# Kernel tuning notes

Hardware: AMD Instinct MI355X
Metric: run time of the kernel (lower is better)

Reference implementation:

```python
import jax, jax.numpy as jnp
import numpy as np

ALPHA = 0.2          # LeakyReLU negative slope
NEG = -9e15          # masking value from the torch source


def _gat_multihead(x, adj, W, a):
    """All nheads GATLayers (concat=True math, elu applied by caller).
    x: [B,N,F], adj: [B,N,N], W: [H,F,O], a: [H,2O]. Returns [B,H,N,O].
    Note a_input @ a decomposes as h_i.a[:O] + h_j.a[O:], so we never
    materialize the O(N^2 * 2O) pairwise concat tensor."""
    h = jnp.einsum('bnf,hfo->bhno', x, W)            # [B,H,N,O]
    O = h.shape[-1]
    s1 = jnp.einsum('bhno,ho->bhn', h, a[:, :O])     # h_i . a_src
    s2 = jnp.einsum('bhno,ho->bhn', h, a[:, O:])     # h_j . a_dst
    e = jax.nn.leaky_relu(s1[..., :, None] + s2[..., None, :], ALPHA)  # [B,H,N,N]
    att = jax.nn.softmax(jnp.where(adj[:, None] > 0, e, NEG), axis=-1)
    return jnp.einsum('bhij,bhjo->bhio', att, h)


def _gat_single(x, adj, W, a):
    """out_att GATLayer (concat=False, no elu). W: [F,O], a: [2O]."""
    h = jnp.einsum('bnf,fo->bno', x, W)
    O = W.shape[-1]
    s1 = h @ a[:O]
    s2 = h @ a[O:]
    e = jax.nn.leaky_relu(s1[:, :, None] + s2[:, None, :], ALPHA)
    att = jax.nn.softmax(jnp.where(adj > 0, e, NEG), axis=-1)
    return jnp.einsum('bij,bjo->bio', att, h)


def setup_inputs() -> dict:
    key = jax.random.key(0)
    ks = jax.random.split(key, 10)
    B, N, F = 2, 2048, 768
    H, O = 8, 256
    x = jax.random.normal(ks[0], (B, N, F), dtype=jnp.float32)
    # sparse-ish binary adjacency (adj>0 is all that matters) + self loops
    adj = (jax.random.uniform(ks[1], (B, N, N)) < 0.05).astype(jnp.float32)
    adj = jnp.maximum(adj, jnp.eye(N, dtype=jnp.float32)[None])
    mask = jnp.ones((B, N, 1), dtype=jnp.float32)  # unused by GAT.forward
    s = 0.05
    W_heads = jax.random.normal(ks[2], (H, F, O), dtype=jnp.float32) * s
    a_heads = jax.random.normal(ks[3], (H, 2 * O), dtype=jnp.float32) * s
    W_out = jax.random.normal(ks[4], (H * O, O), dtype=jnp.float32) * s
    a_out = jax.random.normal(ks[5], (2 * O,), dtype=jnp.float32) * s
    W_lin = jax.random.normal(ks[6], (O, H * O), dtype=jnp.float32) * s  # nn.Linear weight [out,in]
    b_lin = jnp.zeros((O,), dtype=jnp.float32)
    W_ln = jax.random.normal(ks[7], (O, O), dtype=jnp.float32) * s
    b_ln = jnp.zeros((O,), dtype=jnp.float32)
    return {"x": x, "adj": adj, "mask": mask, "W_heads": W_heads,
            "a_heads": a_heads, "W_out": W_out, "a_out": a_out,
            "W_lin": W_lin, "b_lin": b_lin, "W_ln": W_ln, "b_ln": b_ln}


def reference(x, adj, mask, W_heads, a_heads, W_out, a_out, W_lin, b_lin, W_ln, b_ln):
    # layer 0: multi-head GAT, elu, concat over heads (dropout=0 in eval)
    hp = jax.nn.elu(_gat_multihead(x, adj, W_heads, a_heads))  # [B,H,N,O]
    B, H, N, O = hp.shape
    x1 = jnp.transpose(hp, (0, 2, 1, 3)).reshape(B, N, H * O)
    # layer 1: residual linear + out_att (concat=False)
    x2 = x1 @ W_lin.T + b_lin + _gat_single(x1, adj, W_out, a_out)
    # final: relu(ln(x))
    return jax.nn.relu(x2 @ W_ln.T + b_ln)
```

## Files before the change

kernel.cpp:

```cpp
#include <hip/hip_runtime.h>
#include <hip/hip_bf16.h>

constexpr int Bb = 2, Nn = 2048, Ff = 768, Hh = 8, Oo = 256;

typedef __attribute__((ext_vector_type(8)))  short   short8;
typedef __attribute__((ext_vector_type(16))) float   f32x16;
typedef __attribute__((ext_vector_type(4)))  unsigned short ushort4_t;

__device__ inline unsigned short f2bf(float f) {
    unsigned u = __float_as_uint(f);
    u = (u + 0x7FFFu + ((u >> 16) & 1u)) >> 16;
    return (unsigned short)u;
}

__device__ inline void wfrag_kn_body(
        const float* __restrict__ W, unsigned short* __restrict__ out,
        int K, int N, int fblk, int t) {
    int f = fblk * 4 + (t >> 6);
    int slot = t & 63, kh = slot >> 5, lm = slot & 31;
    int nfk = K >> 4;
    int nt = f / nfk, kt = f - nt * nfk;
    const float* wp = W + (size_t)(kt * 16 + kh * 8) * N + nt * 32 + lm;
    ushort4_t o0, o1;
    o0.x = f2bf(wp[0]);             o0.y = f2bf(wp[(size_t)N]);
    o0.z = f2bf(wp[2 * (size_t)N]); o0.w = f2bf(wp[3 * (size_t)N]);
    o1.x = f2bf(wp[4 * (size_t)N]); o1.y = f2bf(wp[5 * (size_t)N]);
    o1.z = f2bf(wp[6 * (size_t)N]); o1.w = f2bf(wp[7 * (size_t)N]);
    unsigned short* op = out + (size_t)f * 512 + slot * 8;
    *(ushort4_t*)op = o0;
    *(ushort4_t*)(op + 4) = o1;
}

__device__ inline void wfrag_nk_body(
        const float* __restrict__ W, unsigned short* __restrict__ out,
        int K, int fblk, int t) {
    int f = fblk * 4 + (t >> 6);
    int slot = t & 63, kh = slot >> 5, lm = slot & 31;
    int nfk = K >> 4;
    int nt = f / nfk, kt = f - nt * nfk;
    const float* wp = W + (size_t)(nt * 32 + lm) * K + kt * 16 + kh * 8;
    float4 a = *(const float4*)wp, b = *(const float4*)(wp + 4);
    ushort4_t o0, o1;
    o0.x = f2bf(a.x); o0.y = f2bf(a.y); o0.z = f2bf(a.z); o0.w = f2bf(a.w);
    o1.x = f2bf(b.x); o1.y = f2bf(b.y); o1.z = f2bf(b.z); o1.w = f2bf(b.w);
    unsigned short* op = out + (size_t)f * 512 + slot * 8;
    *(ushort4_t*)op = o0;
    *(ushort4_t*)(op + 4) = o1;
}

__global__ __launch_bounds__(256) void prep_misc_kernel(
        const float* __restrict__ adj, unsigned long long* __restrict__ bits,
        const float* __restrict__ x, unsigned short* __restrict__ x_bf,
        const float* __restrict__ W_heads, unsigned short* __restrict__ WhF,
        const float* __restrict__ W_out,   unsigned short* __restrict__ WoF,
        const float* __restrict__ W_lin,   unsigned short* __restrict__ WlF,
        const float* __restrict__ W_ln,    unsigned short* __restrict__ WnF) {
    int blk = blockIdx.x, t = threadIdx.x;
    if (blk < 32768) {
        size_t gid = (size_t)blk * 256 + t;
        float v = adj[gid];
        unsigned long long m = __ballot(v > 0.f);
        if ((t & 63) == 0) bits[gid >> 6] = m;
    } else if (blk < 35840) {
        size_t i = (size_t)(blk - 32768) * 256 + t;
        float4 v = ((const float4*)x)[i];
        ushort4_t o;
        o.x = f2bf(v.x); o.y = f2bf(v.y); o.z = f2bf(v.z); o.w = f2bf(v.w);
        ((ushort4_t*)x_bf)[i] = o;
    } else if (blk < 36608) {
        int idx = blk - 35840;
        int head = idx / 96, fblk = idx - head * 96;
        wfrag_kn_body(W_heads + (size_t)head * Ff * Oo, WhF + (size_t)head * 384 * 512,
                      Ff, Oo, fblk, t);
    } else if (blk < 36864) {
        wfrag_kn_body(W_out, WoF, Hh * Oo, Oo, blk - 36608, t);
    } else if (blk < 37120) {
        wfrag_nk_body(W_lin, WlF, Hh * Oo, blk - 36864, t);
    } else {
        wfrag_nk_body(W_ln, WnF, Oo, blk - 37120, t);
    }
}

template<int SWAPZ>
__global__ __launch_bounds__(256) void gemm32_kernel(
        const unsigned short* __restrict__ A, int K, long long sA, int bAshift,
        const unsigned short* __restrict__ BF, long long sB, int bmask,
        float* __restrict__ C, long long sC,
        unsigned short* __restrict__ CF, long long sCF, int Mtot,
        const float* __restrict__ bias, int mode,
        const float* __restrict__ aall, int amask,
        float* __restrict__ E1p, float* __restrict__ E1n, float2* __restrict__ E2pn) {
    int z  = SWAPZ ? blockIdx.x : blockIdx.z;
    int mx = SWAPZ ? blockIdx.y : blockIdx.x;
    A  += (size_t)(z >> bAshift) * sA;
    BF += (size_t)(z & bmask) * sB;
    if (C) C += (size_t)z * sC;
    if (CF) CF += (size_t)z * sCF;
    int m0 = mx * 32;
    int t = threadIdx.x;
    int wv = t >> 6, lane = t & 63;
    int lm = lane & 31, kh = lane >> 5;
    int nfk = K >> 4;
    __shared__ __align__(16) unsigned short As[32][136];
    f32x16 acc[2] = {};
    int sr = t >> 3, sc2 = (t & 7) * 16;
    const unsigned short* ag  = A + (size_t)(m0 + sr) * K + sc2;
    const unsigned short* bg0 = BF + (size_t)(wv * 2) * nfk * 512;
    const unsigned short* bg1 = bg0 + (size_t)nfk * 512;
    for (int k0 = 0; k0 < K; k0 += 128) {
        *(short8*)&As[sr][sc2]     = *(const short8*)(ag + k0);
        *(short8*)&As[sr][sc2 + 8] = *(const short8*)(ag + k0 + 8);
        int kt0 = k0 >> 4;
        __syncthreads();
#pragma unroll
        for (int s = 0; s < 8; ++s) {
            short8 a0 = *(const short8*)&As[lm][s * 16 + kh * 8];
            short8 b0 = *(const short8*)(bg0 + (size_t)(kt0 + s) * 512 + lane * 8);
            short8 b1 = *(const short8*)(bg1 + (size_t)(kt0 + s) * 512 + lane * 8);
            acc[0] = __builtin_amdgcn_mfma_f32_32x32x16_bf16(a0, b0, acc[0], 0, 0, 0);
            acc[1] = __builtin_amdgcn_mfma_f32_32x32x16_bf16(a0, b1, acc[1], 0, 0, 0);
        }
        __syncthreads();
    }
#pragma unroll
    for (int nt = 0; nt < 2; ++nt) {
        int colg = wv * 64 + nt * 32 + lm;
        float bv = (mode == 2) ? bias[colg] : 0.f;
        if (C) {
#pragma unroll
            for (int reg = 0; reg < 16; ++reg) {
                int rl = 4 * kh + (reg & 3) + 8 * (reg >> 2);
                float v = acc[nt][reg];
                if (mode == 2) { v += bv; v = fmaxf(v, 0.f); }
                C[(size_t)(m0 + rl) * 256 + colg] = v;
            }
        }
        if (mode == 1) {
#pragma unroll
            for (int q = 0; q < 4; ++q) {
                int kt = m0 / 16 + (q >> 1);
                size_t fi = ((size_t)(colg >> 5) * (Mtot / 16) + kt) * 512 +
                            ((q & 1) * 32 + (colg & 31)) * 8 + kh * 4;
                ushort4_t pk;
                pk.x = f2bf(acc[nt][q * 4 + 0]);
                pk.y = f2bf(acc[nt][q * 4 + 1]);
                pk.z = f2bf(acc[nt][q * 4 + 2]);
                pk.w = f2bf(acc[nt][q * 4 + 3]);
                *(ushort4_t*)(CF + fi) = pk;
            }
        }
    }
    if (aall) {
        const float* av = aall + (size_t)(z & amask) * 512;
        float a1v0 = av[wv * 64 + lm],       a1v1 = av[wv * 64 + 32 + lm];
        float a2v0 = av[256 + wv * 64 + lm], a2v1 = av[256 + wv * 64 + 32 + lm];
        float* sbuf = (float*)As;
#pragma unroll
        for (int reg = 0; reg < 16; ++reg) {
            int rl = 4 * kh + (reg & 3) + 8 * (reg >> 2);
            float v1 = acc[0][reg] * a1v0 + acc[1][reg] * a1v1;
            float v2 = acc[0][reg] * a2v0 + acc[1][reg] * a2v1;
#pragma unroll
            for (int m = 1; m <= 16; m <<= 1) {
                v1 += __shfl_xor(v1, m, 64);
                v2 += __shfl_xor(v2, m, 64);
            }
            if (lm == 0) { sbuf[rl * 8 + wv] = v1; sbuf[rl * 8 + 4 + wv] = v2; }
        }
        __syncthreads();
        if (t < 32) {
            float s1 = sbuf[t * 8] + sbuf[t * 8 + 1] + sbuf[t * 8 + 2] + sbuf[t * 8 + 3];
            float s2 = sbuf[t * 8 + 4] + sbuf[t * 8 + 5] + sbuf[t * 8 + 6] + sbuf[t * 8 + 7];
            size_t ei = (size_t)z * Nn + m0 + t;
            E1p[ei] = __expf(s1);
            E1n[ei] = __expf(0.2f * s1);
            E2pn[ei] = make_float2(__expf(s2), __expf(0.2f * s2));
        }
    }
}

__global__ __launch_bounds__(512) void gemm32_dual_kernel(
        const unsigned short* __restrict__ A, int K, long long sA,
        const unsigned short* __restrict__ BF,
        unsigned short* __restrict__ h2f, float* __restrict__ lin,
        const float* __restrict__ a_out,
        float* __restrict__ E1p, float* __restrict__ E1n, float2* __restrict__ E2pn) {
    int b = blockIdx.z, ng = blockIdx.y;
    A += (size_t)b * sA;
    int nfk = K >> 4;
    BF += (size_t)ng * 8 * nfk * 512;
    int m0 = blockIdx.x * 32;
    int t = threadIdx.x;
    int wv = t >> 6, lane = t & 63;
    int lm = lane & 31, kh = lane >> 5;
    __shared__ __align__(16) unsigned short As[32][136];
    f32x16 acc = {};
    int sr = t >> 4, sc2 = (t & 15) * 8;
    const unsigned short* ag = A + (size_t)(m0 + sr) * K + sc2;
    const unsigned short* bg = BF + (size_t)wv * nfk * 512;
    for (int k0 = 0; k0 < K; k0 += 128) {
        *(short8*)&As[sr][sc2] = *(const short8*)(ag + k0);
        int kt0 = k0 >> 4;
        __syncthreads();
#pragma unroll
        for (int s = 0; s < 8; ++s) {
            short8 a0 = *(const short8*)&As[lm][s * 16 + kh * 8];
            short8 b0 = *(const short8*)(bg + (size_t)(kt0 + s) * 512 + lane * 8);
            acc = __builtin_amdgcn_mfma_f32_32x32x16_bf16(a0, b0, acc, 0, 0, 0);
        }
        __syncthreads();
    }
    int colg = wv * 32 + lm;
    if (ng == 1) {
        float* C = lin + (size_t)b * Nn * 256;
#pragma unroll
        for (int reg = 0; reg < 16; ++reg) {
            int rl = 4 * kh + (reg & 3) + 8 * (reg >> 2);
            C[(size_t)(m0 + rl) * 256 + colg] = acc[reg];
        }
    } else {
        unsigned short* CF = h2f + (size_t)b * 524288;
#pragma unroll
        for (int q = 0; q < 4; ++q) {
            int kt = m0 / 16 + (q >> 1);
            size_t fi = ((size_t)(colg >> 5) * 128 + kt) * 512 +
                        ((q & 1) * 32 + (colg & 31)) * 8 + kh * 4;
            ushort4_t pk;
            pk.x = f2bf(acc[q * 4 + 0]);
            pk.y = f2bf(acc[q * 4 + 1]);
            pk.z = f2bf(acc[q * 4 + 2]);
            pk.w = f2bf(acc[q * 4 + 3]);
            *(ushort4_t*)(CF + fi) = pk;
        }
        float a1v = a_out[colg];
        float a2v = a_out[256 + colg];
        float* sbuf = (float*)As;
#pragma unroll
        for (int reg = 0; reg < 16; ++reg) {
            int rl = 4 * kh + (reg & 3) + 8 * (reg >> 2);
            float v1 = acc[reg] * a1v;
            float v2 = acc[reg] * a2v;
#pragma unroll
            for (int m = 1; m <= 16; m <<= 1) {
                v1 += __shfl_xor(v1, m, 64);
                v2 += __shfl_xor(v2, m, 64);
            }
            if (lm == 0) { sbuf[rl * 16 + wv] = v1; sbuf[rl * 16 + 8 + wv] = v2; }
        }
        __syncthreads();
        if (t < 32) {
            float s1 = 0.f, s2 = 0.f;
#pragma unroll
            for (int k = 0; k < 8; ++k) {
                s1 += sbuf[t * 16 + k];
                s2 += sbuf[t * 16 + 8 + k];
            }
            size_t ei = (size_t)b * Nn + m0 + t;
            E1p[ei] = __expf(s1);
            E1n[ei] = __expf(0.2f * s1);
            E2pn[ei] = make_float2(__expf(s2), __expf(0.2f * s2));
        }
    }
}

__global__ __launch_bounds__(256) void gemm32_final_kernel(
        const float* __restrict__ pacc, const float* __restrict__ plsum,
        const float* __restrict__ lin, const float* __restrict__ b_lin,
        const unsigned short* __restrict__ BF, const float* __restrict__ b_ln,
        float* __restrict__ out) {
    int b = blockIdx.z, oc = blockIdx.y;
    int m0 = blockIdx.x * 32;
    int t = threadIdx.x;
    int wv = t >> 6, lane = t & 63;
    int lm = lane & 31, kh = lane >> 5;
    constexpr int nfk = 16;
    __shared__ __align__(16) unsigned short As[32][136];
    f32x16 acc = {};
    int sr = t >> 3, sc2 = (t & 7) * 16;
    int row = m0 + sr;
    int BN = Bb * Nn;
    size_t prow = (size_t)b * Nn + row;
    float li = 1.f / (plsum[prow] + plsum[prow + BN] + plsum[prow + 2 * BN] + plsum[prow + 3 * BN]);
    size_t ps4 = (size_t)Bb * Nn * 256;
    const unsigned short* bg = BF + (size_t)(oc * 4 + wv) * nfk * 512;
    for (int k0 = 0; k0 < 256; k0 += 128) {
        int o = k0 + sc2;
        size_t pidx = prow * 256 + o;
#pragma unroll
        for (int g = 0; g < 4; ++g) {
            float4 s4 = *(const float4*)(pacc + pidx + 4 * g);
#pragma unroll
            for (int k = 1; k < 4; ++k) {
                float4 q = *(const float4*)(pacc + k * ps4 + pidx + 4 * g);
                s4.x += q.x; s4.y += q.y; s4.z += q.z; s4.w += q.w;
            }
            float4 lv = *(const float4*)(lin + pidx + 4 * g);
            float4 bv = *(const float4*)(b_lin + o + 4 * g);
            ushort4_t pk;
            pk.x = f2bf(s4.x * li + lv.x + bv.x);
            pk.y = f2bf(s4.y * li + lv.y + bv.y);
            pk.z = f2bf(s4.z * li + lv.z + bv.z);
            pk.w = f2bf(s4.w * li + lv.w + bv.w);
            *(ushort4_t*)&As[sr][sc2 + 4 * g] = pk;
        }
        int kt0 = k0 >> 4;
        __syncthreads();
#pragma unroll
        for (int s = 0; s < 8; ++s) {
            short8 a0 = *(const short8*)&As[lm][s * 16 + kh * 8];
            short8 b0 = *(const short8*)(bg + (size_t)(kt0 + s) * 512 + lane * 8);
            acc = __builtin_amdgcn_mfma_f32_32x32x16_bf16(a0, b0, acc, 0, 0, 0);
        }
        __syncthreads();
    }
    float* C = out + (size_t)b * Nn * 256;
    int colg = oc * 128 + wv * 32 + lm;
    float bv = b_ln[colg];
#pragma unroll
    for (int reg = 0; reg < 16; ++reg) {
        int rl = 4 * kh + (reg & 3) + 8 * (reg >> 2);
        float v = fmaxf(acc[reg] + bv, 0.f);
        C[(size_t)(m0 + rl) * 256 + colg] = v;
    }
}

template<int JLEN, int MODE, int SWAPXY>
__global__ __launch_bounds__(256, 4) void attn_v11_kernel(
        const unsigned short* __restrict__ hfrag,
        const unsigned* __restrict__ bits,
        const float* __restrict__ E1p, const float* __restrict__ E1n,
        const float2* __restrict__ E2pn,
        unsigned short* __restrict__ outbf, int ldo,
        float* __restrict__ pacc, float* __restrict__ plsum,
        int hshift) {
    constexpr int W = JLEN / 32, NC = JLEN / 64, ABS = W + 1;
    int it = SWAPXY ? blockIdx.y : blockIdx.x;
    int bh = SWAPXY ? blockIdx.x : blockIdx.y;
    int js = blockIdx.z;
    int b = bh >> hshift, hd = bh & ((1 << hshift) - 1);
    int i0 = it * 32, jbase = js * JLEN;
    int kt0 = js * (JLEN / 16);
    int t = threadIdx.x, lane = t & 63;
    int wv = t >> 6, lm = lane & 31, kh = lane >> 5;
    int ti = t & 31, jq = t >> 5;

    __shared__ unsigned ab[32 * ABS];
    __shared__ __align__(16) unsigned short ps[2][32][64];
    __shared__ float lred[32][9];
    __shared__ float linv[32];

    const unsigned* bb = bits + ((size_t)b * Nn + i0) * 64 + (jbase >> 5);
    for (int k = t; k < 32 * W; k += 256) {
        int r = k / W, w0 = k - r * W;
        ab[r * ABS + w0] = bb[(size_t)r * 64 + w0];
    }
    __syncthreads();

    float e1p = E1p[(size_t)bh * Nn + i0 + ti];
    float e1n = E1n[(size_t)bh * Nn + i0 + ti];
    const float4* e2base = (const float4*)(E2pn + (size_t)bh * Nn + jbase);

    const unsigned short* bg0 = hfrag + (size_t)bh * 524288 + (size_t)(wv * 2) * 128 * 512;
    const unsigned short* bg1 = bg0 + 128 * 512;

    f32x16 acc[2] = {};
    float lp0 = 0.f, lp1 = 0.f;
    short8 Bpp[4][2];
    float4 e2r[4];

    auto loadE2 = [&](int c) {
        const float4* ep = e2base + ((c * 64 + jq * 8) >> 1);
#pragma unroll
        for (int u = 0; u < 4; ++u) e2r[u] = ep[u];
    };
    auto loadBs = [&](int c, int s, int slot) {
        int kt = kt0 + c * 4 + s;
        Bpp[slot][0] = *(const short8*)(bg0 + (size_t)kt * 512 + lane * 8);
        Bpp[slot][1] = *(const short8*)(bg1 + (size_t)kt * 512 + lane * 8);
    };
    auto computeP = [&](int c, int buf) {
        int cj = c * 64;
        unsigned word = ab[ti * ABS + (cj >> 5) + (jq >> 2)];
        unsigned field = (word >> ((jq & 3) * 8)) & 0xffu;
        unsigned pk[4];
#pragma unroll
        for (int u = 0; u < 4; ++u) {
            float4 q = e2r[u];
            float p0 = fmaxf(e1p * q.x, e1n * q.y);
            p0 = ((field >> (2 * u)) & 1u) ? p0 : 0.f;
            float p1 = fmaxf(e1p * q.z, e1n * q.w);
            p1 = ((field >> (2 * u + 1)) & 1u) ? p1 : 0.f;
            if (u & 1) lp1 += p0 + p1; else lp0 += p0 + p1;
            __hip_bfloat162 hv = __float22bfloat162_rn(make_float2(p0, p1));
            pk[u] = *(unsigned*)&hv;
        }
        uint4 v; v.x = pk[0]; v.y = pk[1]; v.z = pk[2]; v.w = pk[3];
        *(uint4*)&ps[buf][ti][(jq ^ (ti & 7)) * 8] = v;
    };
    auto mfmaS = [&](int buf, int s, int slot) {
        int g = 2 * s + kh;
        short8 a0 = *(const short8*)&ps[buf][lm][(g ^ (lm & 7)) * 8];
        acc[0] = __builtin_amdgcn_mfma_f32_32x32x16_bf16(a0, Bpp[slot][0], acc[0], 0, 0, 0);
        acc[1] = __builtin_amdgcn_mfma_f32_32x32x16_bf16(a0, Bpp[slot][1], acc[1], 0, 0, 0);
    };

    loadE2(0);
    computeP(0, 0);
    loadBs(0, 0, 0); loadBs(0, 1, 1); loadBs(0, 2, 2); loadBs(0, 3, 3);
    __syncthreads();
    for (int c = 0; c < NC; ++c) {
        int cb = c & 1, nb = cb ^ 1;
        bool more = (c + 1 < NC);
        if (more) loadE2(c + 1);
        __builtin_amdgcn_s_setprio(1);
        mfmaS(cb, 0, 0);  if (more) loadBs(c + 1, 0, 0);
        mfmaS(cb, 1, 1);  if (more) loadBs(c + 1, 1, 1);
        mfmaS(cb, 2, 2);  if (more) loadBs(c + 1, 2, 2);
        mfmaS(cb, 3, 3);  if (more) loadBs(c + 1, 3, 3);
        __builtin_amdgcn_s_setprio(0);
        if (more) computeP(c + 1, nb);
        __syncthreads();
    }

    lred[ti][jq] = lp0 + lp1;
    __syncthreads();
    if (MODE == 0) {
        if (t < 32) {
            float s = 0.f;
#pragma unroll
            for (int k = 0; k < 8; ++k) s += lred[t][k];
            linv[t] = 1.f / s;
        }
        __syncthreads();
#pragma unroll
        for (int nt = 0; nt < 2; ++nt) {
            int o = wv * 64 + nt * 32 + lm;
#pragma unroll
            for (int reg = 0; reg < 16; ++reg) {
                int rl = 4 * kh + (reg & 3) + 8 * (reg >> 2);
                float v = acc[nt][reg] * linv[rl];
                v = v > 0.f ? v : expm1f(v);
                outbf[((size_t)b * Nn + i0 + rl) * ldo + (size_t)hd * Oo + o] = f2bf(v);
            }
        }
    } else {
        if (t < 32) {
            float s = 0.f;
#pragma unroll
            for (int k = 0; k < 8; ++k) s += lred[t][k];
            plsum[((size_t)js * Bb + b) * Nn + i0 + t] = s;
        }
        float* pa = pacc + (((size_t)js * Bb + b) * Nn) * 256;
#pragma unroll
        for (int nt = 0; nt < 2; ++nt) {
            int o = wv * 64 + nt * 32 + lm;
#pragma unroll
            for (int reg = 0; reg < 16; ++reg) {
                int rl = 4 * kh + (reg & 3) + 8 * (reg >> 2);
                pa[(size_t)(i0 + rl) * 256 + o] = acc[nt][reg];
            }
        }
    }
}

extern "C" void kernel_launch(void* const* d_in, const int* in_sizes, int n_in,
                              void* d_out, int out_size, void* d_ws, size_t ws_size,
                              hipStream_t stream) {
    const float* x       = (const float*)d_in[0];
    const float* adj     = (const float*)d_in[1];
    const float* W_heads = (const float*)d_in[3];
    const float* a_heads = (const float*)d_in[4];
    const float* W_out   = (const float*)d_in[5];
    const float* a_out   = (const float*)d_in[6];
    const float* W_lin   = (const float*)d_in[7];
    const float* b_lin   = (const float*)d_in[8];
    const float* W_ln    = (const float*)d_in[9];
    const float* b_ln    = (const float*)d_in[10];

    char* w = (char*)d_ws;
    float* pacc     = (float*)(w);
    float* lin      = (float*)(w + 33554432);
    float* E1p_mh   = (float*)(w + 41943040);
    float* E1n_mh   = (float*)(w + 42074112);
    float2* E2pn_mh = (float2*)(w + 42205184);
    float* E1p_sh   = (float*)(w + 42467328);
    float* E1n_sh   = (float*)(w + 42483712);
    float2* E2pn_sh = (float2*)(w + 42500096);
    unsigned long long* bits = (unsigned long long*)(w + 42532864);
    unsigned short* x_bf  = (unsigned short*)(w + 43581440);
    unsigned short* WhF   = (unsigned short*)(w + 49872896);
    unsigned short* WoF   = (unsigned short*)(w + 53018624);
    unsigned short* WlF   = (unsigned short*)(w + 54067200);
    unsigned short* WnF   = (unsigned short*)(w + 55115776);
    unsigned short* hfrag = (unsigned short*)(w + 55246848);
    unsigned short* h2frag= (unsigned short*)(w + 72024064);
    unsigned short* x1_bf = (unsigned short*)(w + 74121216);
    float* plsum = E1p_mh;

    prep_misc_kernel<<<37152, 256, 0, stream>>>(
        adj, bits, x, x_bf, W_heads, WhF, W_out, WoF, W_lin, WlF, W_ln, WnF);

    gemm32_kernel<1><<<dim3(Bb * Hh, Nn / 32, 1), 256, 0, stream>>>(
        x_bf, Ff, (long long)Nn * Ff, 3, WhF, 384LL * 512, 7,
        nullptr, 0, hfrag, 524288, Nn, nullptr, 1,
        a_heads, 7, E1p_mh, E1n_mh, E2pn_mh);
    attn_v11_kernel<2048, 0, 1><<<dim3(Bb * Hh, Nn / 32, 1), 256, 0, stream>>>(
        hfrag, (const unsigned*)bits, E1p_mh, E1n_mh, E2pn_mh,
        x1_bf, Hh * Oo, nullptr, nullptr, 3);
    gemm32_dual_kernel<<<dim3(Nn / 32, 2, Bb), 512, 0, stream>>>(
        x1_bf, Hh * Oo, (long long)Nn * Hh * Oo, WoF, h2frag, lin,
        a_out, E1p_sh, E1n_sh, E2pn_sh);
    attn_v11_kernel<512, 1, 0><<<dim3(Nn / 32, Bb, 4), 256, 0, stream>>>(
        h2frag, (const unsigned*)bits, E1p_sh, E1n_sh, E2pn_sh,
        nullptr, 0, pacc, plsum, 0);
    gemm32_final_kernel<<<dim3(Nn / 32, 2, Bb), 256, 0, stream>>>(
        pacc, plsum, lin, b_lin, WnF, b_ln, (float*)d_out);
}
```

Baseline: 253.5 us.

## Double-buffer GEMM A tiles, deepen attention pipeline, split single-head attention eightfold

The three GEMM kernels now use two LDS buffers for the A tile and prefetch the next tile into registers, which removes one barrier per K step. The attention kernel keeps four probability buffers and computes two chunks ahead, giving more latency hiding between MFMA and softmax-weight computation. The single-head attention's J dimension is split 8 ways instead of 4 to raise parallelism, and the final kernel sums 8 partials. This adds LDS use and partial-sum traffic, and it assumes NC is even.

```diff
diff --git a/kernel.cpp b/kernel.cpp
--- a/kernel.cpp
+++ b/kernel.cpp
@@ -2,6 +2,7 @@
 #include <hip/hip_bf16.h>
 
 constexpr int Bb = 2, Nn = 2048, Ff = 768, Hh = 8, Oo = 256;
+constexpr int NSPLIT = 8;
 
 typedef __attribute__((ext_vector_type(8)))  short   short8;
 typedef __attribute__((ext_vector_type(16))) float   f32x16;
@@ -101,26 +102,33 @@
     int wv = t >> 6, lane = t & 63;
     int lm = lane & 31, kh = lane >> 5;
     int nfk = K >> 4;
-    __shared__ __align__(16) unsigned short As[32][136];
+    __shared__ __align__(16) unsigned short As[2][32][136];
     f32x16 acc[2] = {};
     int sr = t >> 3, sc2 = (t & 7) * 16;
     const unsigned short* ag  = A + (size_t)(m0 + sr) * K + sc2;
     const unsigned short* bg0 = BF + (size_t)(wv * 2) * nfk * 512;
     const unsigned short* bg1 = bg0 + (size_t)nfk * 512;
+    short8 r0 = *(const short8*)(ag);
+    short8 r1 = *(const short8*)(ag + 8);
+    int cur = 0;
     for (int k0 = 0; k0 < K; k0 += 128) {
-        *(short8*)&As[sr][sc2]     = *(const short8*)(ag + k0);
-        *(short8*)&As[sr][sc2 + 8] = *(const short8*)(ag + k0 + 8);
+        *(short8*)&As[cur][sr][sc2]     = r0;
+        *(short8*)&As[cur][sr][sc2 + 8] = r1;
+        __syncthreads();
+        if (k0 + 128 < K) {
+            r0 = *(const short8*)(ag + k0 + 128);
+            r1 = *(const short8*)(ag + k0 + 136);
+        }
         int kt0 = k0 >> 4;
-        __syncthreads();
 #pragma unroll
         for (int s = 0; s < 8; ++s) {
-            short8 a0 = *(const short8*)&As[lm][s * 16 + kh * 8];
+            short8 a0 = *(const short8*)&As[cur][lm][s * 16 + kh * 8];
             short8 b0 = *(const short8*)(bg0 + (size_t)(kt0 + s) * 512 + lane * 8);
             short8 b1 = *(const short8*)(bg1 + (size_t)(kt0 + s) * 512 + lane * 8);
             acc[0] = __builtin_amdgcn_mfma_f32_32x32x16_bf16(a0, b0, acc[0], 0, 0, 0);
             acc[1] = __builtin_amdgcn_mfma_f32_32x32x16_bf16(a0, b1, acc[1], 0, 0, 0);
         }
-        __syncthreads();
+        cur ^= 1;
     }
 #pragma unroll
     for (int nt = 0; nt < 2; ++nt) {
@@ -151,6 +159,7 @@
         }
     }
     if (aall) {
+        __syncthreads();
         const float* av = aall + (size_t)(z & amask) * 512;
         float a1v0 = av[wv * 64 + lm],       a1v1 = av[wv * 64 + 32 + lm];
         float a2v0 = av[256 + wv * 64 + lm], a2v1 = av[256 + wv * 64 + 32 + lm];
@@ -193,22 +202,25 @@
     int t = threadIdx.x;
     int wv = t >> 6, lane = t & 63;
     int lm = lane & 31, kh = lane >> 5;
-    __shared__ __align__(16) unsigned short As[32][136];
+    __shared__ __align__(16) unsigned short As[2][32][136];
     f32x16 acc = {};
     int sr = t >> 4, sc2 = (t & 15) * 8;
     const unsigned short* ag = A + (size_t)(m0 + sr) * K + sc2;
     const unsigned short* bg = BF + (size_t)wv * nfk * 512;
+    short8 r = *(const short8*)(ag);
+    int cur = 0;
     for (int k0 = 0; k0 < K; k0 += 128) {
-        *(short8*)&As[sr][sc2] = *(const short8*)(ag + k0);
+        *(short8*)&As[cur][sr][sc2] = r;
+        __syncthreads();
+        if (k0 + 128 < K) r = *(const short8*)(ag + k0 + 128);
         int kt0 = k0 >> 4;
-        __syncthreads();
 #pragma unroll
         for (int s = 0; s < 8; ++s) {
-            short8 a0 = *(const short8*)&As[lm][s * 16 + kh * 8];
+            short8 a0 = *(const short8*)&As[cur][lm][s * 16 + kh * 8];
             short8 b0 = *(const short8*)(bg + (size_t)(kt0 + s) * 512 + lane * 8);
             acc = __builtin_amdgcn_mfma_f32_32x32x16_bf16(a0, b0, acc, 0, 0, 0);
         }
-        __syncthreads();
+        cur ^= 1;
     }
     int colg = wv * 32 + lm;
     if (ng == 1) {
@@ -232,6 +244,7 @@
             pk.w = f2bf(acc[q * 4 + 3]);
             *(ushort4_t*)(CF + fi) = pk;
         }
+        __syncthreads();
         float a1v = a_out[colg];
         float a2v = a_out[256 + colg];
         float* sbuf = (float*)As;
@@ -274,23 +287,28 @@
     int wv = t >> 6, lane = t & 63;
     int lm = lane & 31, kh = lane >> 5;
     constexpr int nfk = 16;
-    __shared__ __align__(16) unsigned short As[32][136];
+    __shared__ __align__(16) unsigned short As[2][32][136];
     f32x16 acc = {};
     int sr = t >> 3, sc2 = (t & 7) * 16;
     int row = m0 + sr;
     int BN = Bb * Nn;
     size_t prow = (size_t)b * Nn + row;
-    float li = 1.f / (plsum[prow] + plsum[prow + BN] + plsum[prow + 2 * BN] + plsum[prow + 3 * BN]);
+    float ls = 0.f;
+#pragma unroll
+    for (int k = 0; k < NSPLIT; ++k) ls += plsum[prow + k * BN];
+    float li = 1.f / ls;
     size_t ps4 = (size_t)Bb * Nn * 256;
     const unsigned short* bg = BF + (size_t)(oc * 4 + wv) * nfk * 512;
-    for (int k0 = 0; k0 < 256; k0 += 128) {
+
+    ushort4_t stage[4];
+    auto computePK = [&](int k0) {
         int o = k0 + sc2;
         size_t pidx = prow * 256 + o;
 #pragma unroll
         for (int g = 0; g < 4; ++g) {
             float4 s4 = *(const float4*)(pacc + pidx + 4 * g);
 #pragma unroll
-            for (int k = 1; k < 4; ++k) {
+            for (int k = 1; k < NSPLIT; ++k) {
                 float4 q = *(const float4*)(pacc + k * ps4 + pidx + 4 * g);
                 s4.x += q.x; s4.y += q.y; s4.z += q.z; s4.w += q.w;
             }
@@ -301,17 +319,25 @@
             pk.y = f2bf(s4.y * li + lv.y + bv.y);
             pk.z = f2bf(s4.z * li + lv.z + bv.z);
             pk.w = f2bf(s4.w * li + lv.w + bv.w);
-            *(ushort4_t*)&As[sr][sc2 + 4 * g] = pk;
-        }
+            stage[g] = pk;
+        }
+    };
+    computePK(0);
+    int cur = 0;
+    for (int k0 = 0; k0 < 256; k0 += 128) {
+#pragma unroll
+        for (int g = 0; g < 4; ++g)
+            *(ushort4_t*)&As[cur][sr][sc2 + 4 * g] = stage[g];
+        __syncthreads();
+        if (k0 == 0) computePK(128);
         int kt0 = k0 >> 4;
-        __syncthreads();
 #pragma unroll
         for (int s = 0; s < 8; ++s) {
-            short8 a0 = *(const short8*)&As[lm][s * 16 + kh * 8];
+            short8 a0 = *(const short8*)&As[cur][lm][s * 16 + kh * 8];
             short8 b0 = *(const short8*)(bg + (size_t)(kt0 + s) * 512 + lane * 8);
             acc = __builtin_amdgcn_mfma_f32_32x32x16_bf16(a0, b0, acc, 0, 0, 0);
         }
-        __syncthreads();
+        cur ^= 1;
     }
     float* C = out + (size_t)b * Nn * 256;
     int colg = oc * 128 + wv * 32 + lm;
@@ -325,7 +351,7 @@
 }
 
 template<int JLEN, int MODE, int SWAPXY>
-__global__ __launch_bounds__(256, 4) void attn_v11_kernel(
+__global__ __launch_bounds__(256, 4) void attn_v12_kernel(
         const unsigned short* __restrict__ hfrag,
         const unsigned* __restrict__ bits,
         const float* __restrict__ E1p, const float* __restrict__ E1n,
@@ -345,7 +371,7 @@
     int ti = t & 31, jq = t >> 5;
 
     __shared__ unsigned ab[32 * ABS];
-    __shared__ __align__(16) unsigned short ps[2][32][64];
+    __shared__ __align__(16) unsigned short ps[4][32][64];
     __shared__ float lred[32][9];
     __shared__ float linv[32];
 
@@ -366,26 +392,25 @@
     f32x16 acc[2] = {};
     float lp0 = 0.f, lp1 = 0.f;
     short8 Bpp[4][2];
-    float4 e2r[4];
-
-    auto loadE2 = [&](int c) {
+    float4 e2a[4], e2b[4];
+
+    auto abw = [&](int c) { return ab[ti * ABS + c * 2 + (jq >> 2)]; };
+    auto loadE2 = [&](int c, float4 (&e2)[4]) {
         const float4* ep = e2base + ((c * 64 + jq * 8) >> 1);
 #pragma unroll
-        for (int u = 0; u < 4; ++u) e2r[u] = ep[u];
+        for (int u = 0; u < 4; ++u) e2[u] = ep[u];
     };
     auto loadBs = [&](int c, int s, int slot) {
         int kt = kt0 + c * 4 + s;
         Bpp[slot][0] = *(const short8*)(bg0 + (size_t)kt * 512 + lane * 8);
         Bpp[slot][1] = *(const short8*)(bg1 + (size_t)kt * 512 + lane * 8);
     };
-    auto computeP = [&](int c, int buf) {
-        int cj = c * 64;
-        unsigned word = ab[ti * ABS + (cj >> 5) + (jq >> 2)];
+    auto computeP = [&](int buf, const float4 (&e2)[4], unsigned word) {
         unsigned field = (word >> ((jq & 3) * 8)) & 0xffu;
         unsigned pk[4];
 #pragma unroll
         for (int u = 0; u < 4; ++u) {
-            float4 q = e2r[u];
+            float4 q = e2[u];
             float p0 = fmaxf(e1p * q.x, e1n * q.y);
             p0 = ((field >> (2 * u)) & 1u) ? p0 : 0.f;
             float p1 = fmaxf(e1p * q.z, e1n * q.w);
@@ -404,21 +429,31 @@
         acc[1] = __builtin_amdgcn_mfma_f32_32x32x16_bf16(a0, Bpp[slot][1], acc[1], 0, 0, 0);
     };
 
-    loadE2(0);
-    computeP(0, 0);
+    loadE2(0, e2a); loadE2(1, e2b);
     loadBs(0, 0, 0); loadBs(0, 1, 1); loadBs(0, 2, 2); loadBs(0, 3, 3);
+    computeP(0, e2a, abw(0));
+    computeP(1, e2b, abw(1));
     __syncthreads();
-    for (int c = 0; c < NC; ++c) {
-        int cb = c & 1, nb = cb ^ 1;
-        bool more = (c + 1 < NC);
-        if (more) loadE2(c + 1);
+
+    for (int c = 0; c < NC; c += 2) {
+        bool m2 = (c + 2 < NC), m3 = (c + 3 < NC);
+        unsigned w2 = m2 ? abw(c + 2) : 0u;
+        unsigned w3 = m3 ? abw(c + 3) : 0u;
+        if (m2) loadE2(c + 2, e2a);
+        if (m3) loadE2(c + 3, e2b);
+        int b0 = c & 3, b1 = (c + 1) & 3;
         __builtin_amdgcn_s_setprio(1);
-        mfmaS(cb, 0, 0);  if (more) loadBs(c + 1, 0, 0);
-        mfmaS(cb, 1, 1);  if (more) loadBs(c + 1, 1, 1);
-        mfmaS(cb, 2, 2);  if (more) loadBs(c + 1, 2, 2);
-        mfmaS(cb, 3, 3);  if (more) loadBs(c + 1, 3, 3);
+        mfmaS(b0, 0, 0);  loadBs(c + 1, 0, 0);
+        mfmaS(b0, 1, 1);  loadBs(c + 1, 1, 1);
+        mfmaS(b0, 2, 2);  loadBs(c + 1, 2, 2);
+        mfmaS(b0, 3, 3);  loadBs(c + 1, 3, 3);
+        mfmaS(b1, 0, 0);  if (m2) loadBs(c + 2, 0, 0);
+        mfmaS(b1, 1, 1);  if (m2) loadBs(c + 2, 1, 1);
+        mfmaS(b1, 2, 2);  if (m2) loadBs(c + 2, 2, 2);
+        mfmaS(b1, 3, 3);  if (m2) loadBs(c + 2, 3, 3);
         __builtin_amdgcn_s_setprio(0);
-        if (more) computeP(c + 1, nb);
+        if (m2) computeP((c + 2) & 3, e2a, w2);
+        if (m3) computeP((c + 3) & 3, e2b, w3);
         __syncthreads();
     }
 
@@ -504,13 +539,13 @@
         x_bf, Ff, (long long)Nn * Ff, 3, WhF, 384LL * 512, 7,
         nullptr, 0, hfrag, 524288, Nn, nullptr, 1,
         a_heads, 7, E1p_mh, E1n_mh, E2pn_mh);
-    attn_v11_kernel<2048, 0, 1><<<dim3(Bb * Hh, Nn / 32, 1), 256, 0, stream>>>(
+    attn_v12_kernel<2048, 0, 1><<<dim3(Bb * Hh, Nn / 32, 1), 256, 0, stream>>>(
         hfrag, (const unsigned*)bits, E1p_mh, E1n_mh, E2pn_mh,
         x1_bf, Hh * Oo, nullptr, nullptr, 3);
     gemm32_dual_kernel<<<dim3(Nn / 32, 2, Bb), 512, 0, stream>>>(
         x1_bf, Hh * Oo, (long long)Nn * Hh * Oo, WoF, h2frag, lin,
         a_out, E1p_sh, E1n_sh, E2pn_sh);
-    attn_v11_kernel<512, 1, 0><<<dim3(Nn / 32, Bb, 4), 256, 0, stream>>>(
+    attn_v12_kernel<256, 1, 0><<<dim3(Nn / 32, Bb, NSPLIT), 256, 0, stream>>>(
         h2frag, (const unsigned*)bits, E1p_sh, E1n_sh, E2pn_sh,
         nullptr, 0, pacc, plsum, 0);
     gemm32_final_kernel<<<dim3(Nn / 32, 2, Bb), 256, 0, stream>>>(
```

Measured after the change: 291.5 us. +15.0%, slower.
